# Kernel tuning notes

Hardware: AMD Instinct MI355X
Metric: run time of the kernel (lower is better)

## Reference

```python
import jax, jax.numpy as jnp
import numpy as np

N = 20        # number_of_nodes
K = 2         # Chebyshev order
E_DIM = 4     # embedding_dimensions
OUT = 2       # out_channels
F_IN = 8      # node_features
B = 131072    # batch


def setup_inputs() -> dict:
    key = jax.random.key(0)
    ks = jax.random.split(key, 8)
    x = jax.random.normal(ks[0], (B, N, F_IN), jnp.float32)
    e = jax.random.normal(ks[1], (N, E_DIM), jnp.float32)
    # AVWGCN parameter pools: weights_pool (E_DIM, K, in, out), bias_pool (E_DIM, out)
    gate_w = jax.random.normal(ks[2], (E_DIM, K, F_IN + OUT, 2 * OUT), jnp.float32) * 0.1
    gate_b = jax.random.normal(ks[3], (E_DIM, 2 * OUT), jnp.float32) * 0.1
    upd_w = jax.random.normal(ks[4], (E_DIM, K, F_IN + OUT, OUT), jnp.float32) * 0.1
    upd_b = jax.random.normal(ks[5], (E_DIM, OUT), jnp.float32) * 0.1
    lin_w = jax.random.normal(ks[6], (1, OUT), jnp.float32) * 0.5
    lin_b = jax.random.normal(ks[7], (1,), jnp.float32) * 0.1
    return {"x": x, "e": e, "gate_w": gate_w, "gate_b": gate_b,
            "upd_w": upd_w, "upd_b": upd_b, "lin_w": lin_w, "lin_b": lin_b}


def _avwgcn(x, e, supports, w_pool, b_pool):
    # Node-adaptive weights: (N, K, in, out) and bias (N, out)
    W = jnp.einsum('nd,dkio->nkio', e, w_pool)
    b = e @ b_pool
    # K-hop graph conv gather: (B, N, K, in)
    x_g = jnp.einsum('knm,bmc->bnkc', supports, x)
    return jnp.einsum('bnki,nkio->bno', x_g, W) + b


def reference(x, e, gate_w, gate_b, upd_w, upd_b, lin_w, lin_b):
    dt = x.dtype
    # Adaptive adjacency: softmax(relu(E E^T)) rows; Chebyshev set for K=2 is [I, A]
    A = jax.nn.softmax(jax.nn.relu(e @ e.T), axis=1)
    supports = jnp.stack([jnp.eye(N, dtype=dt), A.astype(dt)])  # (K, N, N)

    H = jnp.zeros((x.shape[0], N, OUT), dt)  # self.h is None -> zeros
    XH = jnp.concatenate([x, H], axis=-1)
    ZR = jax.nn.sigmoid(_avwgcn(XH, e, supports, gate_w, gate_b))
    Z, R = ZR[..., :OUT], ZR[..., OUT:]
    C = jnp.concatenate([x, Z * H], axis=-1)
    HC = jnp.tanh(_avwgcn(C, e, supports, upd_w, upd_b))
    H = R * H + (1.0 - R) * HC

    y = jax.nn.relu(H)
    y = y @ lin_w.T + lin_b
    return y
```

## Files before the change

kernel.cpp:

```cpp
#include <hip/hip_runtime.h>
#include <math.h>

#define NN 20
#define ED 4
#define XROW 160
#define NC 80
#define NKT 5
#define NNT 5
#define FRAG_BYTES (NKT * NNT * 64 * 16)
#define BIAS_OFF   FRAG_BYTES
#define LIN_OFF    (BIAS_OFF + NC * 4)
#define CONS_BYTES (LIN_OFF + 16)
#define CONS_U4    (CONS_BYTES / 16)
#define THREADS 512
#define ROWS_PER_WAVE 16
#define ROWS_PER_BLOCK 128
#define EPI_STRIDE 84

typedef __attribute__((ext_vector_type(8))) _Float16 half8;
typedef __attribute__((ext_vector_type(4))) float f32x4;
typedef __attribute__((ext_vector_type(4))) unsigned uint4v;

static __device__ __forceinline__ half8 cvt8(float4 a, float4 b) {
    half8 r;
    r[0] = (_Float16)a.x; r[1] = (_Float16)a.y; r[2] = (_Float16)a.z; r[3] = (_Float16)a.w;
    r[4] = (_Float16)b.x; r[5] = (_Float16)b.y; r[6] = (_Float16)b.z; r[7] = (_Float16)b.w;
    return r;
}

__global__ void rgcn_setup(const float* __restrict__ e,
                           const float* __restrict__ gate_w,
                           const float* __restrict__ gate_b,
                           const float* __restrict__ upd_w,
                           const float* __restrict__ upd_b,
                           const float* __restrict__ lin_w,
                           const float* __restrict__ lin_b,
                           char* __restrict__ ws) {
    __shared__ float el[80];
    __shared__ float sA[400];
    __shared__ float wself[640];
    __shared__ float wagg[640];
    const int t = threadIdx.x;
    const int l = t & 63;
    const int w = t >> 6;

    if (t < NN * ED) el[t] = e[t];
    __syncthreads();

    if (t < 400) {
        int n = t / 20, m = t - (t / 20) * 20;
        float d = 0.f;
        for (int j = 0; j < ED; ++j) d += el[n * ED + j] * el[m * ED + j];
        sA[t] = fmaxf(d, 0.f);
    }
    for (int idx = t; idx < 1280; idx += THREADS) {
        int sel = idx >= 640;
        int rem = sel ? idx - 640 : idx;
        int c = rem >> 3, i = rem & 7;
        int n = c >> 2, ro = c & 3;
        float v = 0.f;
        if (ro < 2) {
            int o = 2 + ro;
            for (int d = 0; d < ED; ++d) v += el[n * ED + d] * gate_w[d * 80 + sel * 40 + i * 4 + o];
        } else {
            int o = ro - 2;
            for (int d = 0; d < ED; ++d) v += el[n * ED + d] * upd_w[d * 40 + sel * 20 + i * 2 + o];
        }
        (sel ? wagg : wself)[rem] = v;
    }
    float* wbias = (float*)(ws + BIAS_OFF);
    float* wlin  = (float*)(ws + LIN_OFF);
    if (t < NC) {
        int n = t >> 2, ro = t & 3;
        float b = 0.f;
        for (int d = 0; d < ED; ++d)
            b += el[n * ED + d] * (ro < 2 ? gate_b[d * 4 + 2 + ro] : upd_b[d * 2 + ro - 2]);
        wbias[t] = b;
    }
    if (t == 0) { wlin[0] = lin_w[0]; wlin[1] = lin_w[1]; wlin[2] = lin_b[0]; wlin[3] = 0.f; }
    __syncthreads();

    if (t < NN) {
        float mx = -1e30f;
        for (int m = 0; m < NN; ++m) mx = fmaxf(mx, sA[t * 20 + m]);
        float ex[NN]; float sum = 0.f;
        for (int m = 0; m < NN; ++m) { ex[m] = __expf(sA[t * 20 + m] - mx); sum += ex[m]; }
        float inv = 1.f / sum;
        for (int m = 0; m < NN; ++m) sA[t * 20 + m] = ex[m] * inv;
    }
    __syncthreads();

    half8* frag = (half8*)ws;
    for (int tile = w; tile < NKT * NNT; tile += (THREADS / 64)) {
        int kt = tile / 5, nt = tile - kt * 5;
        int c = nt * 16 + (l & 15);
        int n = c >> 2;
        int m = kt * 4 + (l >> 4);
        float anm = sA[n * 20 + m];
        float4 wg0 = *(const float4*)&wagg[c * 8];
        float4 wg1 = *(const float4*)&wagg[c * 8 + 4];
        float v0 = anm * wg0.x, v1 = anm * wg0.y, v2 = anm * wg0.z, v3 = anm * wg0.w;
        float v4 = anm * wg1.x, v5 = anm * wg1.y, v6 = anm * wg1.z, v7 = anm * wg1.w;
        if (n == m) {
            float4 ws0 = *(const float4*)&wself[c * 8];
            float4 ws1 = *(const float4*)&wself[c * 8 + 4];
            v0 += ws0.x; v1 += ws0.y; v2 += ws0.z; v3 += ws0.w;
            v4 += ws1.x; v5 += ws1.y; v6 += ws1.z; v7 += ws1.w;
        }
        half8 hv;
        hv[0] = (_Float16)v0; hv[1] = (_Float16)v1; hv[2] = (_Float16)v2; hv[3] = (_Float16)v3;
        hv[4] = (_Float16)v4; hv[5] = (_Float16)v5; hv[6] = (_Float16)v6; hv[7] = (_Float16)v7;
        frag[tile * 64 + l] = hv;
    }
}

__global__ __launch_bounds__(THREADS, 6) void rgcn_main(
        const float* __restrict__ x,
        const char* __restrict__ cons,
        float* __restrict__ y) {
    __shared__ __align__(16) char smem[CONS_BYTES];
    const int t = threadIdx.x;
    const int l = t & 63;
    const int w = t >> 6;

    const size_t row0 = (size_t)blockIdx.x * ROWS_PER_BLOCK + (size_t)w * ROWS_PER_WAVE;
    const float* xp = x + (row0 + (l & 15)) * XROW + ((l >> 4) << 3);
    float4 xa0 = *(const float4*)(xp);       float4 xb0 = *(const float4*)(xp + 4);
    float4 xa1 = *(const float4*)(xp + 32);  float4 xb1 = *(const float4*)(xp + 36);
    float4 xa2 = *(const float4*)(xp + 64);  float4 xb2 = *(const float4*)(xp + 68);
    float4 xa3 = *(const float4*)(xp + 96);  float4 xb3 = *(const float4*)(xp + 100);
    float4 xa4 = *(const float4*)(xp + 128); float4 xb4 = *(const float4*)(xp + 132);

    {
        const uint4v* src = (const uint4v*)cons;
        uint4v* dst = (uint4v*)smem;
        #pragma unroll
        for (int i = t; i < CONS_U4; i += THREADS) dst[i] = src[i];
    }
    __syncthreads();

    const half8* frag = (const half8*)smem;
    const float* sbias = (const float*)(smem + BIAS_OFF);
    const float* slin  = (const float*)(smem + LIN_OFF);

    f32x4 acc[NNT];
    #pragma unroll
    for (int nt = 0; nt < NNT; ++nt) acc[nt] = (f32x4){0.f, 0.f, 0.f, 0.f};

    #define STEP(XA, XB, KT)                                                        \
    {                                                                               \
        half8 a = cvt8(XA, XB);                                                     \
        _Pragma("unroll")                                                           \
        for (int nt = 0; nt < NNT; ++nt) {                                          \
            half8 bh = frag[((KT) * NNT + nt) * 64 + l];                            \
            acc[nt] = __builtin_amdgcn_mfma_f32_16x16x32_f16(a, bh, acc[nt], 0, 0, 0); \
        }                                                                           \
    }
    STEP(xa0, xb0, 0)
    STEP(xa1, xb1, 1)
    STEP(xa2, xb2, 2)
    STEP(xa3, xb3, 3)
    STEP(xa4, xb4, 4)
    #undef STEP

    const float lw0 = slin[0], lw1 = slin[1], lb = slin[2];
    __syncthreads();
    float* epi = (float*)smem;
    #pragma unroll
    for (int qb = 0; qb < 4; qb += 2) {
        #pragma unroll
        for (int nt = 0; nt < NNT; ++nt) {
            int c = nt * 16 + (l & 15);
            float bia = sbias[c];
            #pragma unroll
            for (int dq = 0; dq < 2; ++dq) {
                int rc = w * 8 + ((l >> 4) << 1) + dq;
                epi[rc * EPI_STRIDE + c] = acc[nt][qb + dq] + bia;
            }
        }
        __syncthreads();
        #pragma unroll
        for (int o = t; o < 64 * NN; o += THREADS) {
            int rc = o / 20;
            int n = o - rc * 20;
            float4 p = *(const float4*)&epi[rc * EPI_STRIDE + n * 4];
            float e0 = __expf(p.x);
            float e1 = __expf(p.y);
            float i0 = __builtin_amdgcn_rcpf(1.f + e0);
            float i1 = __builtin_amdgcn_rcpf(1.f + e1);
            float t0 = 1.f - 2.f * __builtin_amdgcn_rcpf(__expf(2.f * p.z) + 1.f);
            float t1 = 1.f - 2.f * __builtin_amdgcn_rcpf(__expf(2.f * p.w) + 1.f);
            float h0 = i0 * t0;
            float h1 = i1 * t1;
            float yv = fmaxf(h0, 0.f) * lw0 + fmaxf(h1, 0.f) * lw1 + lb;
            size_t g = (size_t)blockIdx.x * ROWS_PER_BLOCK
                     + (size_t)(rc >> 3) * ROWS_PER_WAVE
                     + (((rc & 7) >> 1) << 2) + qb + (rc & 1);
            y[g * NN + n] = yv;
        }
        __syncthreads();
    }
}

extern "C" void kernel_launch(void* const* d_in, const int* in_sizes, int n_in,
                              void* d_out, int out_size, void* d_ws, size_t ws_size,
                              hipStream_t stream) {
    const float* x      = (const float*)d_in[0];
    const float* e      = (const float*)d_in[1];
    const float* gate_w = (const float*)d_in[2];
    const float* gate_b = (const float*)d_in[3];
    const float* upd_w  = (const float*)d_in[4];
    const float* upd_b  = (const float*)d_in[5];
    const float* lin_w  = (const float*)d_in[6];
    const float* lin_b  = (const float*)d_in[7];
    char* cons = (char*)d_ws;
    float* y   = (float*)d_out;

    const int Bn = in_sizes[0] / XROW;
    const int nblocks = Bn / ROWS_PER_BLOCK;

    rgcn_setup<<<1, THREADS, 0, stream>>>(e, gate_w, gate_b, upd_w, upd_b,
                                          lin_w, lin_b, cons);
    rgcn_main<<<nblocks, THREADS, 0, stream>>>(x, cons, y);
}
```

Before: 26.18 us.

## Compute GRU epilogue in registers via DPP shuffles instead of LDS round-trip

Replaces the shared-memory epilogue (store accumulators, barrier, re-read per node) with a register-only epilogue that folds bias into the accumulator init and uses DPP lane swaps to combine R and tanh terms and the two output channels. It also converts x to fp16 with packed cvt_pkrtz instructions, and restructures the setup kernel to 640 threads so each thread computes one weight element, with parameter loads hoisted before the first barrier. This removes two block barriers and LDS traffic in the main kernel, at the cost of redundant transcendental work across lanes and scattered 4-byte stores.

```diff
diff --git a/kernel.cpp b/kernel.cpp
--- a/kernel.cpp
+++ b/kernel.cpp
@@ -13,29 +13,41 @@
 #define CONS_BYTES (LIN_OFF + 16)
 #define CONS_U4    (CONS_BYTES / 16)
 #define THREADS 512
+#define STH 640
 #define ROWS_PER_WAVE 16
 #define ROWS_PER_BLOCK 128
-#define EPI_STRIDE 84
 
 typedef __attribute__((ext_vector_type(8))) _Float16 half8;
 typedef __attribute__((ext_vector_type(4))) float f32x4;
 typedef __attribute__((ext_vector_type(4))) unsigned uint4v;
 
 static __device__ __forceinline__ half8 cvt8(float4 a, float4 b) {
-    half8 r;
-    r[0] = (_Float16)a.x; r[1] = (_Float16)a.y; r[2] = (_Float16)a.z; r[3] = (_Float16)a.w;
-    r[4] = (_Float16)b.x; r[5] = (_Float16)b.y; r[6] = (_Float16)b.z; r[7] = (_Float16)b.w;
-    return r;
-}
-
-__global__ void rgcn_setup(const float* __restrict__ e,
-                           const float* __restrict__ gate_w,
-                           const float* __restrict__ gate_b,
-                           const float* __restrict__ upd_w,
-                           const float* __restrict__ upd_b,
-                           const float* __restrict__ lin_w,
-                           const float* __restrict__ lin_b,
-                           char* __restrict__ ws) {
+    uint4v u = (uint4v){
+        __builtin_bit_cast(unsigned, __builtin_amdgcn_cvt_pkrtz(a.x, a.y)),
+        __builtin_bit_cast(unsigned, __builtin_amdgcn_cvt_pkrtz(a.z, a.w)),
+        __builtin_bit_cast(unsigned, __builtin_amdgcn_cvt_pkrtz(b.x, b.y)),
+        __builtin_bit_cast(unsigned, __builtin_amdgcn_cvt_pkrtz(b.z, b.w))};
+    return __builtin_bit_cast(half8, u);
+}
+
+static __device__ __forceinline__ float dpp_xor1(float v) {
+    return __builtin_bit_cast(float,
+        __builtin_amdgcn_mov_dpp(__builtin_bit_cast(int, v), 0xB1, 0xF, 0xF, true));
+}
+static __device__ __forceinline__ float dpp_xor2(float v) {
+    return __builtin_bit_cast(float,
+        __builtin_amdgcn_mov_dpp(__builtin_bit_cast(int, v), 0x4E, 0xF, 0xF, true));
+}
+
+__global__ __launch_bounds__(STH) void rgcn_setup(
+        const float* __restrict__ e,
+        const float* __restrict__ gate_w,
+        const float* __restrict__ gate_b,
+        const float* __restrict__ upd_w,
+        const float* __restrict__ upd_b,
+        const float* __restrict__ lin_w,
+        const float* __restrict__ lin_b,
+        char* __restrict__ ws) {
     __shared__ float el[80];
     __shared__ float sA[400];
     __shared__ float wself[640];
@@ -44,40 +56,54 @@
     const int l = t & 63;
     const int w = t >> 6;
 
-    if (t < NN * ED) el[t] = e[t];
-    __syncthreads();
-
-    if (t < 400) {
-        int n = t / 20, m = t - (t / 20) * 20;
-        float d = 0.f;
-        for (int j = 0; j < ED; ++j) d += el[n * ED + j] * el[m * ED + j];
-        sA[t] = fmaxf(d, 0.f);
-    }
-    for (int idx = t; idx < 1280; idx += THREADS) {
-        int sel = idx >= 640;
-        int rem = sel ? idx - 640 : idx;
-        int c = rem >> 3, i = rem & 7;
-        int n = c >> 2, ro = c & 3;
-        float v = 0.f;
-        if (ro < 2) {
-            int o = 2 + ro;
-            for (int d = 0; d < ED; ++d) v += el[n * ED + d] * gate_w[d * 80 + sel * 40 + i * 4 + o];
-        } else {
-            int o = ro - 2;
-            for (int d = 0; d < ED; ++d) v += el[n * ED + d] * upd_w[d * 40 + sel * 20 + i * 2 + o];
-        }
-        (sel ? wagg : wself)[rem] = v;
-    }
+    const int c = t >> 3, i = t & 7;
+    const int n_ = c >> 2, ro = c & 3;
+    float p0[4], p1[4];
+    {
+        const float* b0;
+        const float* b1;
+        int st;
+        if (ro < 2) { b0 = gate_w + i * 4 + 2 + ro; b1 = b0 + 40; st = 80; }
+        else        { b0 = upd_w  + i * 2 + ro - 2; b1 = b0 + 20; st = 40; }
+        #pragma unroll
+        for (int d = 0; d < ED; ++d) { p0[d] = b0[d * st]; p1[d] = b1[d * st]; }
+    }
+    float pb[4];
+    if (t < NC) {
+        int rb = t & 3;
+        #pragma unroll
+        for (int d = 0; d < ED; ++d)
+            pb[d] = (rb < 2) ? gate_b[d * 4 + 2 + rb] : upd_b[d * 2 + rb - 2];
+    }
+    if (t < 80) el[t] = e[t];
     float* wbias = (float*)(ws + BIAS_OFF);
     float* wlin  = (float*)(ws + LIN_OFF);
+    if (t == 0) { wlin[0] = lin_w[0]; wlin[1] = lin_w[1]; wlin[2] = lin_b[0]; wlin[3] = 0.f; }
+    __syncthreads();
+
+    if (t < 400) {
+        int nn = t / 20, mm = t - (t / 20) * 20;
+        float d = 0.f;
+        for (int j = 0; j < ED; ++j) d += el[nn * ED + j] * el[mm * ED + j];
+        sA[t] = fmaxf(d, 0.f);
+    }
+    {
+        float vs = 0.f, va = 0.f;
+        #pragma unroll
+        for (int d = 0; d < ED; ++d) {
+            float ev = el[n_ * ED + d];
+            vs += ev * p0[d];
+            va += ev * p1[d];
+        }
+        wself[t] = vs;
+        wagg[t]  = va;
+    }
     if (t < NC) {
-        int n = t >> 2, ro = t & 3;
         float b = 0.f;
-        for (int d = 0; d < ED; ++d)
-            b += el[n * ED + d] * (ro < 2 ? gate_b[d * 4 + 2 + ro] : upd_b[d * 2 + ro - 2]);
+        #pragma unroll
+        for (int d = 0; d < ED; ++d) b += el[(t >> 2) * ED + d] * pb[d];
         wbias[t] = b;
     }
-    if (t == 0) { wlin[0] = lin_w[0]; wlin[1] = lin_w[1]; wlin[2] = lin_b[0]; wlin[3] = 0.f; }
     __syncthreads();
 
     if (t < NN) {
@@ -91,19 +117,19 @@
     __syncthreads();
 
     half8* frag = (half8*)ws;
-    for (int tile = w; tile < NKT * NNT; tile += (THREADS / 64)) {
+    for (int tile = w; tile < NKT * NNT; tile += (STH / 64)) {
         int kt = tile / 5, nt = tile - kt * 5;
-        int c = nt * 16 + (l & 15);
-        int n = c >> 2;
-        int m = kt * 4 + (l >> 4);
-        float anm = sA[n * 20 + m];
-        float4 wg0 = *(const float4*)&wagg[c * 8];
-        float4 wg1 = *(const float4*)&wagg[c * 8 + 4];
+        int cc = nt * 16 + (l & 15);
+        int nn = cc >> 2;
+        int mm = kt * 4 + (l >> 4);
+        float anm = sA[nn * 20 + mm];
+        float4 wg0 = *(const float4*)&wagg[cc * 8];
+        float4 wg1 = *(const float4*)&wagg[cc * 8 + 4];
         float v0 = anm * wg0.x, v1 = anm * wg0.y, v2 = anm * wg0.z, v3 = anm * wg0.w;
         float v4 = anm * wg1.x, v5 = anm * wg1.y, v6 = anm * wg1.z, v7 = anm * wg1.w;
-        if (n == m) {
-            float4 ws0 = *(const float4*)&wself[c * 8];
-            float4 ws1 = *(const float4*)&wself[c * 8 + 4];
+        if (nn == mm) {
+            float4 ws0 = *(const float4*)&wself[cc * 8];
+            float4 ws1 = *(const float4*)&wself[cc * 8 + 4];
             v0 += ws0.x; v1 += ws0.y; v2 += ws0.z; v3 += ws0.w;
             v4 += ws1.x; v5 += ws1.y; v6 += ws1.z; v7 += ws1.w;
         }
@@ -145,7 +171,10 @@
 
     f32x4 acc[NNT];
     #pragma unroll
-    for (int nt = 0; nt < NNT; ++nt) acc[nt] = (f32x4){0.f, 0.f, 0.f, 0.f};
+    for (int nt = 0; nt < NNT; ++nt) {
+        float b = sbias[nt * 16 + (l & 15)];
+        acc[nt] = (f32x4){b, b, b, b};
+    }
 
     #define STEP(XA, XB, KT)                                                        \
     {                                                                               \
@@ -164,41 +193,31 @@
     #undef STEP
 
     const float lw0 = slin[0], lw1 = slin[1], lb = slin[2];
-    __syncthreads();
-    float* epi = (float*)smem;
+    const int ro = l & 3;
+    const bool isR = ro < 2;
+    const float myw = (ro & 1) ? lw1 : lw0;
+    const size_t rowb = row0 + ((l >> 4) << 2) + ro;
+
     #pragma unroll
-    for (int qb = 0; qb < 4; qb += 2) {
-        #pragma unroll
-        for (int nt = 0; nt < NNT; ++nt) {
-            int c = nt * 16 + (l & 15);
-            float bia = sbias[c];
-            #pragma unroll
-            for (int dq = 0; dq < 2; ++dq) {
-                int rc = w * 8 + ((l >> 4) << 1) + dq;
-                epi[rc * EPI_STRIDE + c] = acc[nt][qb + dq] + bia;
+    for (int nt = 0; nt < NNT; ++nt) {
+        const int n = nt * 4 + ((l & 15) >> 2);
+        float ysel = 0.f;
+        #pragma unroll
+        for (int q = 0; q < 4; ++q) {
+            float pre = acc[nt][q];
+            float term;
+            if (isR) {
+                term = __builtin_amdgcn_rcpf(1.f + __expf(pre));
+            } else {
+                term = 1.f - 2.f * __builtin_amdgcn_rcpf(__expf(2.f * pre) + 1.f);
             }
+            float other = dpp_xor2(term);
+            float h = term * other;
+            float s = fmaxf(h, 0.f) * myw;
+            float yq = s + dpp_xor1(s) + lb;
+            if (q == ro) ysel = yq;
         }
-        __syncthreads();
-        #pragma unroll
-        for (int o = t; o < 64 * NN; o += THREADS) {
-            int rc = o / 20;
-            int n = o - rc * 20;
-            float4 p = *(const float4*)&epi[rc * EPI_STRIDE + n * 4];
-            float e0 = __expf(p.x);
-            float e1 = __expf(p.y);
-            float i0 = __builtin_amdgcn_rcpf(1.f + e0);
-            float i1 = __builtin_amdgcn_rcpf(1.f + e1);
-            float t0 = 1.f - 2.f * __builtin_amdgcn_rcpf(__expf(2.f * p.z) + 1.f);
-            float t1 = 1.f - 2.f * __builtin_amdgcn_rcpf(__expf(2.f * p.w) + 1.f);
-            float h0 = i0 * t0;
-            float h1 = i1 * t1;
-            float yv = fmaxf(h0, 0.f) * lw0 + fmaxf(h1, 0.f) * lw1 + lb;
-            size_t g = (size_t)blockIdx.x * ROWS_PER_BLOCK
-                     + (size_t)(rc >> 3) * ROWS_PER_WAVE
-                     + (((rc & 7) >> 1) << 2) + qb + (rc & 1);
-            y[g * NN + n] = yv;
-        }
-        __syncthreads();
+        y[rowb * NN + n] = ysel;
     }
 }
 
@@ -219,7 +238,7 @@
     const int Bn = in_sizes[0] / XROW;
     const int nblocks = Bn / ROWS_PER_BLOCK;
 
-    rgcn_setup<<<1, THREADS, 0, stream>>>(e, gate_w, gate_b, upd_w, upd_b,
-                                          lin_w, lin_b, cons);
+    rgcn_setup<<<1, STH, 0, stream>>>(e, gate_w, gate_b, upd_w, upd_b,
+                                      lin_w, lin_b, cons);
     rgcn_main<<<nblocks, THREADS, 0, stream>>>(x, cons, y);
 }
```

Result: slower. 26.90 us (+2.7%).
